# Optimization experiments

Hardware: AMD Instinct MI355X
Metric: run time of the kernel (lower is better)

Reference implementation:

```python
import jax, jax.numpy as jnp
import numpy as np

B, S, HID = 2, 2048, 2048
NH, NKV, HD = 16, 4, 128
G = NH // NKV  # kv group size
EPS = 1e-6


def setup_inputs() -> dict:
    key = jax.random.key(0)
    ks = jax.random.split(key, 7)
    w = 0.02
    return {
        "hidden_states": jax.random.normal(ks[0], (B, S, HID), dtype=jnp.float32),
        "position_ids": jnp.broadcast_to(jnp.arange(S, dtype=jnp.int64), (B, S)),
        "Wq": jax.random.normal(ks[1], (2 * NH * HD, HID), dtype=jnp.float32) * w,
        "Wk": jax.random.normal(ks[2], (NKV * HD, HID), dtype=jnp.float32) * w,
        "Wv": jax.random.normal(ks[3], (NKV * HD, HID), dtype=jnp.float32) * w,
        "Wo": jax.random.normal(ks[4], (HID, NH * HD), dtype=jnp.float32) * w,
        "norm_w": jnp.zeros((HID,), dtype=jnp.float32),
    }


def reference(hidden_states, position_ids, Wq, Wk, Wv, Wo, norm_w):
    # RMSNorm (weight parameterized as 1 + w, per source)
    ms = jnp.mean(hidden_states * hidden_states, axis=-1, keepdims=True)
    x = hidden_states * jax.lax.rsqrt(ms + EPS) * (1.0 + norm_w)

    qg = x @ Wq.T                                   # (B,S,2*NH*HD)
    q, gate = jnp.split(qg, 2, axis=-1)
    q = q.reshape(B, S, NH, HD).transpose(0, 2, 1, 3)       # (B,NH,S,HD)
    gate = gate.reshape(B, S, NH, HD).transpose(0, 2, 1, 3)
    k = (x @ Wk.T).reshape(B, S, NKV, HD).transpose(0, 2, 1, 3)  # (B,NKV,S,HD)
    v = (x @ Wv.T).reshape(B, S, NKV, HD).transpose(0, 2, 1, 3)

    scale = 1.0 / np.sqrt(HD).astype(np.float32)
    qg4 = q.reshape(B, NKV, G, S, HD)
    attn = jnp.einsum("bkgqd,bkld->bkgql", qg4, k) * scale   # (B,NKV,G,S,S)
    p = jax.nn.softmax(attn, axis=-1)
    o = jnp.einsum("bkgql,bkld->bkgqd", p, v).reshape(B, NH, S, HD)

    o = o * jax.nn.sigmoid(gate)                    # output gate
    o = o.transpose(0, 2, 1, 3).reshape(B, S, NH * HD)
    return o @ Wo.T
```

## Files before the change

kernel.cpp:

```cpp
#include <hip/hip_runtime.h>
#include <math.h>

#define BB    2
#define SS    2048
#define HIDD  2048
#define NHH   16
#define NKVV  4
#define HDD   128
#define MROWS 4096
#define QG_N  4096
#define KV_N  512
#define O_N   2048
#define KDIM  2048
#define EPS_  1e-6f
#define SCALE_ 0.08838834764831845f

typedef __attribute__((ext_vector_type(8))) __bf16 bf16x8;
typedef __attribute__((ext_vector_type(8))) unsigned short u16x8;
typedef __attribute__((ext_vector_type(4))) float f32x4;

__device__ __forceinline__ unsigned short f2bf(float f) {
  return __builtin_bit_cast(unsigned short, (__bf16)f);
}

__global__ __launch_bounds__(256) void f2bf_all(const float* __restrict__ Wq,
                                                const float* __restrict__ Wk,
                                                const float* __restrict__ Wv,
                                                const float* __restrict__ Wo,
                                                unsigned short* __restrict__ dst) {
  const int s0 = QG_N * KDIM / 4;
  const int s1 = s0 + KV_N * KDIM / 4;
  const int s2 = s1 + KV_N * KDIM / 4;
  const int s3 = s2 + O_N * KDIM / 4;
  int i = blockIdx.x * 256 + threadIdx.x;
  if (i >= s3) return;
  float4 v;
  if (i < s0)      v = ((const float4*)Wq)[i];
  else if (i < s1) v = ((const float4*)Wk)[i - s0];
  else if (i < s2) v = ((const float4*)Wv)[i - s1];
  else             v = ((const float4*)Wo)[i - s2];
  ushort4 u;
  u.x = f2bf(v.x); u.y = f2bf(v.y); u.z = f2bf(v.z); u.w = f2bf(v.w);
  ((ushort4*)dst)[i] = u;
}

__global__ __launch_bounds__(256) void rmsnorm_k(const float* __restrict__ h,
                                                 const float* __restrict__ w,
                                                 unsigned short* __restrict__ x) {
  int row = blockIdx.x;
  int t = threadIdx.x;
  const float4* hr = (const float4*)(h + (size_t)row * HIDD);
  const float4* w4 = (const float4*)w;

  float4 v0 = hr[t], v1 = hr[t + 256];
  float ss = v0.x*v0.x + v0.y*v0.y + v0.z*v0.z + v0.w*v0.w
           + v1.x*v1.x + v1.y*v1.y + v1.z*v1.z + v1.w*v1.w;
#pragma unroll
  for (int off = 32; off > 0; off >>= 1) ss += __shfl_down(ss, off, 64);

  __shared__ float part[4];
  __shared__ float rs_sh;
  if ((t & 63) == 0) part[t >> 6] = ss;
  __syncthreads();
  if (t == 0) rs_sh = rsqrtf((part[0]+part[1]+part[2]+part[3]) * (1.0f/HIDD) + EPS_);
  __syncthreads();
  float rs = rs_sh;

  float4 w0 = w4[t], w1 = w4[t + 256];
  ushort4 o0, o1;
  o0.x = f2bf(v0.x * rs * (1.f + w0.x));
  o0.y = f2bf(v0.y * rs * (1.f + w0.y));
  o0.z = f2bf(v0.z * rs * (1.f + w0.z));
  o0.w = f2bf(v0.w * rs * (1.f + w0.w));
  o1.x = f2bf(v1.x * rs * (1.f + w1.x));
  o1.y = f2bf(v1.y * rs * (1.f + w1.y));
  o1.z = f2bf(v1.z * rs * (1.f + w1.z));
  o1.w = f2bf(v1.w * rs * (1.f + w1.w));
  ushort4* xr = (ushort4*)(x + (size_t)row * HIDD);
  xr[t] = o0;
  xr[t + 256] = o1;
}

template <int OBF>
__device__ __forceinline__ void gemm_core(const unsigned short* __restrict__ Ab,
                                          const unsigned short* __restrict__ Bb,
                                          void* __restrict__ Cv,
                                          int Ndim, int bm, int bn,
                                          unsigned short* Als, unsigned short* Bls) {
  char* ldsA = (char*)Als;
  char* ldsB = (char*)Bls;

  int t   = threadIdx.x;
  int r15 = t & 15;
  int g   = (t & 63) >> 4;
  int w   = t >> 6;
  int wr  = w >> 1, wc = w & 1;

  f32x4 acc[4][4] = {};

  for (int k0 = 0; k0 < KDIM; k0 += 64) {
    __syncthreads();
#pragma unroll
    for (int it = 0; it < 4; ++it) {
      int f      = it * 256 + t;
      int row    = f >> 3;
      int schunk = (f & 7) ^ (row & 7);
      unsigned ldsbase = (unsigned)((it * 256 + (w << 6)) << 4);
      __builtin_amdgcn_global_load_lds(
          (const unsigned int*)(Ab + ((size_t)(bm + row) << 11) + k0 + schunk * 8),
          (unsigned int*)(ldsA + ldsbase), 16, 0, 0);
      __builtin_amdgcn_global_load_lds(
          (const unsigned int*)(Bb + ((size_t)(bn + row) << 11) + k0 + schunk * 8),
          (unsigned int*)(ldsB + ldsbase), 16, 0, 0);
    }
    __syncthreads();

#pragma unroll
    for (int tt = 0; tt < 2; ++tt) {
      bf16x8 af[4], bfv[4];
#pragma unroll
      for (int mi = 0; mi < 4; ++mi) {
        int row = wr * 64 + mi * 16 + r15;
        af[mi] = *(const bf16x8*)(ldsA + row * 128 + (((4 * tt + g) ^ (row & 7)) << 4));
      }
#pragma unroll
      for (int ni = 0; ni < 4; ++ni) {
        int row = wc * 64 + ni * 16 + r15;
        bfv[ni] = *(const bf16x8*)(ldsB + row * 128 + (((4 * tt + g) ^ (row & 7)) << 4));
      }
      __builtin_amdgcn_s_setprio(1);
#pragma unroll
      for (int mi = 0; mi < 4; ++mi)
#pragma unroll
        for (int ni = 0; ni < 4; ++ni)
          acc[mi][ni] = __builtin_amdgcn_mfma_f32_16x16x32_bf16(af[mi], bfv[ni], acc[mi][ni], 0, 0, 0);
      __builtin_amdgcn_s_setprio(0);
    }
  }

#pragma unroll
  for (int mi = 0; mi < 4; ++mi)
#pragma unroll
    for (int ni = 0; ni < 4; ++ni) {
      int col = bn + wc * 64 + ni * 16 + r15;
#pragma unroll
      for (int r = 0; r < 4; ++r) {
        int rowg = bm + wr * 64 + mi * 16 + g * 4 + r;
        if (OBF == 1)
          ((unsigned short*)Cv)[(size_t)rowg * Ndim + col] = f2bf(acc[mi][ni][r]);
        else if (OBF == 3) {
          int t6 = rowg & 63;
          int sig = (t6 & 32) + ((t6 & 12) << 1) + ((t6 & 16) >> 2) + (t6 & 3);
          int tokp = (rowg & ~63) | sig;
          ((unsigned short*)Cv)[(size_t)col * MROWS + tokp] = f2bf(acc[mi][ni][r]);
        } else
          ((float*)Cv)[(size_t)rowg * Ndim + col] = acc[mi][ni][r];
      }
    }
}

template <int OBF>
__global__ __launch_bounds__(256) void gemm_bf16(const unsigned short* __restrict__ Ab,
                                                 const unsigned short* __restrict__ Bb,
                                                 void* __restrict__ Cv,
                                                 int Ndim) {
  __shared__ unsigned short Als[128 * 64];
  __shared__ unsigned short Bls[128 * 64];
  gemm_core<OBF>(Ab, Bb, Cv, Ndim, blockIdx.y * 128, blockIdx.x * 128, Als, Bls);
}

__global__ __launch_bounds__(256) void gemm_kv(const unsigned short* __restrict__ Ab,
                                               const unsigned short* __restrict__ Wk,
                                               const unsigned short* __restrict__ Wv,
                                               unsigned short* __restrict__ Ck,
                                               unsigned short* __restrict__ Cvt) {
  __shared__ unsigned short Als[128 * 64];
  __shared__ unsigned short Bls[128 * 64];
  int bx = blockIdx.x;
  if (bx < 4)
    gemm_core<1>(Ab, Wk, (void*)Ck, KV_N, blockIdx.y * 128, bx * 128, Als, Bls);
  else
    gemm_core<3>(Ab, Wv, (void*)Cvt, KV_N, blockIdx.y * 128, (bx & 3) * 128, Als, Bls);
}

#define LD8(basep, r, x) \
  (*(const bf16x8*)((basep) + (size_t)(r) * 128 + ((((x) ^ ((r)&7))) << 4)))

#define STAGE_A(bufi, h, tk)                                                   \
  { _Pragma("unroll")                                                          \
    for (int c = 0; c < 2; ++c) {                                              \
      int f = c * 512 + t;                                                     \
      int rr = f >> 3;                                                         \
      int sc = (f & 7) ^ (rr & 7);                                             \
      __builtin_amdgcn_global_load_lds(                                        \
        (const unsigned int*)(Ab + ((size_t)(bm + (h)*128 + rr) << 11) + (tk)*64 + sc*8), \
        (unsigned int*)(lds8 + (bufi)*32768 + (h)*16384 + c*8192 + (w<<10)), 16, 0, 0); \
    } }

#define STAGE_B(bufi, h, tk)                                                   \
  { _Pragma("unroll")                                                          \
    for (int c = 0; c < 2; ++c) {                                              \
      int f = c * 512 + t;                                                     \
      int rr = f >> 3;                                                         \
      int sc = (f & 7) ^ (rr & 7);                                             \
      __builtin_amdgcn_global_load_lds(                                        \
        (const unsigned int*)(Bbp + ((size_t)(bn + (h)*128 + rr) << 11) + (tk)*64 + sc*8), \
        (unsigned int*)(lds8 + 65536 + (bufi)*32768 + (h)*16384 + c*8192 + (w<<10)), 16, 0, 0); \
    } }

#define RD_A(SRC, MIBASE)                                                      \
  { _Pragma("unroll")                                                          \
    for (int mi = 0; mi < 4; ++mi) {                                           \
      int rr = wr * 128 + ((MIBASE) + mi) * 16 + r15;                          \
      afr[mi][0] = LD8(SRC, rr, g);                                            \
      afr[mi][1] = LD8(SRC, rr, 4 + g);                                        \
    } }

#define RD_B(SRC, NIBASE, DST)                                                 \
  { _Pragma("unroll")                                                          \
    for (int ni = 0; ni < 2; ++ni) {                                           \
      int rr = wc * 64 + ((NIBASE) + ni) * 16 + r15;                           \
      DST[ni][0] = LD8(SRC, rr, g);                                            \
      DST[ni][1] = LD8(SRC, rr, 4 + g);                                        \
    } }

#define MFMA_QUAD(MIBASE, NIBASE, BREG)                                        \
  { __builtin_amdgcn_s_setprio(1);                                             \
    _Pragma("unroll")                                                          \
    for (int mi = 0; mi < 4; ++mi)                                             \
      _Pragma("unroll")                                                        \
      for (int ni = 0; ni < 2; ++ni)                                           \
        _Pragma("unroll")                                                      \
        for (int ks = 0; ks < 2; ++ks)                                         \
          acc[(MIBASE)+mi][(NIBASE)+ni] =                                      \
            __builtin_amdgcn_mfma_f32_16x16x32_bf16(afr[mi][ks], BREG[ni][ks], \
                                                    acc[(MIBASE)+mi][(NIBASE)+ni], 0, 0, 0); \
    __builtin_amdgcn_s_setprio(0); }

#define BAR() __builtin_amdgcn_s_barrier()

__global__ __launch_bounds__(512, 2) void gemm_qg256(const unsigned short* __restrict__ Ab,
                                                     const unsigned short* __restrict__ Bbp,
                                                     unsigned short* __restrict__ Cq,
                                                     float* __restrict__ Cg) {
  __shared__ char lds8[131072];
  int t = threadIdx.x;
  int r15 = t & 15, g = (t & 63) >> 4, w = t >> 6;
  int wr = w >> 2, wc = w & 3;
  int bm = blockIdx.y * 256, bn = blockIdx.x * 256;
  char* A0 = lds8;            char* A1 = lds8 + 32768;
  char* B0 = lds8 + 65536;    char* B1 = lds8 + 98304;

  f32x4 acc[8][4] = {};
  bf16x8 afr[4][2], b0r[2][2], b1r[2][2];

  STAGE_A(0, 0, 0); STAGE_A(0, 1, 0); STAGE_B(0, 0, 0); STAGE_B(0, 1, 0);
  STAGE_A(1, 0, 1); STAGE_A(1, 1, 1); STAGE_B(1, 0, 1); STAGE_B(1, 1, 1);
  asm volatile("s_waitcnt vmcnt(8)" ::: "memory");
  BAR();

  for (int i = 0; i < 15; ++i) {
    int te = 2 * i + 2, to = 2 * i + 3;
    RD_A(A0, 0); RD_B(B0, 0, b0r);
    BAR(); MFMA_QUAD(0, 0, b0r); BAR();
    RD_B(B0, 2, b1r);
    BAR(); MFMA_QUAD(0, 2, b1r); BAR();
    RD_A(A0, 4);
    STAGE_B(0, 0, te);
    BAR(); MFMA_QUAD(4, 0, b0r); BAR();
    STAGE_A(0, 0, te);
    BAR(); MFMA_QUAD(4, 2, b1r);
    asm volatile("s_waitcnt vmcnt(4)" ::: "memory");
    BAR();
    RD_A(A1, 0); RD_B(B1, 0, b0r);
    STAGE_A(0, 1, te);
    BAR(); MFMA_QUAD(0, 0, b0r); BAR();
    RD_B(B1, 2, b1r);
    STAGE_B(0, 1, te);
    BAR(); MFMA_QUAD(0, 2, b1r); BAR();
    RD_A(A1, 4);
    STAGE_B(1, 0, to); STAGE_B(1, 1, to);
    BAR(); MFMA_QUAD(4, 0, b0r); BAR();
    STAGE_A(1, 0, to); STAGE_A(1, 1, to);
    BAR(); MFMA_QUAD(4, 2, b1r);
    asm volatile("s_waitcnt vmcnt(8)" ::: "memory");
    BAR();
  }
  RD_A(A0, 0); RD_B(B0, 0, b0r);
  BAR(); MFMA_QUAD(0, 0, b0r); BAR();
  RD_B(B0, 2, b1r);
  BAR(); MFMA_QUAD(0, 2, b1r); BAR();
  RD_A(A0, 4);
  BAR(); MFMA_QUAD(4, 0, b0r); BAR();
  BAR(); MFMA_QUAD(4, 2, b1r);
  asm volatile("s_waitcnt vmcnt(0)" ::: "memory");
  BAR();
  RD_A(A1, 0); RD_B(B1, 0, b0r);
  BAR(); MFMA_QUAD(0, 0, b0r); BAR();
  RD_B(B1, 2, b1r);
  BAR(); MFMA_QUAD(0, 2, b1r); BAR();
  RD_A(A1, 4);
  BAR(); MFMA_QUAD(4, 0, b0r); BAR();
  BAR(); MFMA_QUAD(4, 2, b1r);

  bool isq = (bn < O_N);
  int colbase = bn + wc * 64;
#pragma unroll
  for (int mi = 0; mi < 8; ++mi) {
    size_t row = (size_t)bm + wr * 128 + mi * 16 + g * 4;
#pragma unroll
    for (int ni = 0; ni < 4; ++ni) {
      int col = colbase + ni * 16 + r15;
#pragma unroll
      for (int r = 0; r < 4; ++r) {
        if (isq) Cq[(row + r) * O_N + col] = f2bf(acc[mi][ni][r] * SCALE_);
        else     Cg[(row + r) * O_N + (col - O_N)] = acc[mi][ni][r];
      }
    }
  }
}

__global__ __launch_bounds__(256, 2) void attn_mfma(const unsigned short* __restrict__ qb,
                                                    const float* __restrict__ gateb,
                                                    const unsigned short* __restrict__ kb,
                                                    const unsigned short* __restrict__ vt,
                                                    unsigned short* __restrict__ obuf) {
  __shared__ unsigned short Ks[2][64 * 128];
  __shared__ unsigned short Vt[2][128 * 64];
  char* ldsK0 = (char*)Ks;
  char* ldsV0 = (char*)Vt;

  int t = threadIdx.x;
  int l = t & 63, w = t >> 6;
  int c15 = l & 15, g = l >> 4;
  int bid = blockIdx.x;
  int swz = (bid & 7) * 64 + (bid >> 3);
  int qt = swz & 15, h = (swz >> 4) & 15, b = swz >> 8;
  int kh = h >> 2;
  size_t rowQ0 = (size_t)b * SS + (size_t)qt * 128;
  size_t rowKbase = (size_t)b * SS;

  bf16x8 qf[2][4];
#pragma unroll
  for (int qi = 0; qi < 2; ++qi)
#pragma unroll
    for (int ks = 0; ks < 4; ++ks)
      qf[qi][ks] = *(const bf16x8*)(qb + (rowQ0 + w * 32 + qi * 16 + c15) * O_N
                                       + h * HDD + g * 8 + ks * 32);

  f32x4 accO[2][8] = {};
  float mrun[2] = {-INFINITY, -INFINITY};
  float lrun[2] = {0.f, 0.f};

#define ISSUE_K(bufi, kt_)                                                     \
  {                                                                            \
    size_t rowK0 = rowKbase + (size_t)(kt_) * 64;                              \
    _Pragma("unroll")                                                          \
    for (int it = 0; it < 4; ++it) {                                           \
      int f = it * 256 + t;                                                    \
      int kv = f >> 4;                                                         \
      int schunk = (f & 15) ^ (kv & 7);                                        \
      unsigned ldsbase = (unsigned)((it * 256 + (w << 6)) << 4);               \
      __builtin_amdgcn_global_load_lds(                                        \
          (const unsigned int*)(kb + (rowK0 + kv) * KV_N + kh * HDD + schunk * 8), \
          (unsigned int*)(ldsK0 + (bufi) * 16384 + ldsbase), 16, 0, 0);        \
    }                                                                          \
  }
#define ISSUE_VT(bufi, kt_)                                                    \
  {                                                                            \
    size_t tokbase = rowKbase + (size_t)(kt_) * 64;                            \
    _Pragma("unroll")                                                          \
    for (int it = 0; it < 4; ++it) {                                           \
      int f = it * 256 + t;                                                    \
      int row = f >> 3;                                                        \
      int schunk = (f & 7) ^ (row & 7);                                        \
      unsigned ldsbase = (unsigned)((it * 256 + (w << 6)) << 4);               \
      __builtin_amdgcn_global_load_lds(                                        \
          (const unsigned int*)(vt + (size_t)(kh * 128 + row) * MROWS + tokbase + schunk * 8), \
          (unsigned int*)(ldsV0 + (bufi) * 16384 + ldsbase), 16, 0, 0);        \
    }                                                                          \
  }

  ISSUE_K(0, 0);
  ISSUE_VT(0, 0);
  asm volatile("s_waitcnt vmcnt(0)" ::: "memory");
  __syncthreads();

  const int NT = SS / 64;
  for (int kt = 0; kt < NT; ++kt) {
    int cur = kt & 1, nxt = cur ^ 1;
    char* ldsK = ldsK0 + cur * 16384;
    char* ldsV = ldsV0 + cur * 16384;

    if (kt + 1 < NT) {
      ISSUE_K(nxt, kt + 1);
      ISSUE_VT(nxt, kt + 1);
    }

    f32x4 accS[2][4] = {};
    __builtin_amdgcn_s_setprio(1);
#pragma unroll
    for (int nf = 0; nf < 4; ++nf) {
      int kvr = nf * 16 + c15;
#pragma unroll
      for (int ks = 0; ks < 4; ++ks) {
        bf16x8 kf = *(const bf16x8*)(ldsK + kvr * 256 + ((((g + 4 * ks) ^ (kvr & 7)) << 4)));
#pragma unroll
        for (int qi = 0; qi < 2; ++qi)
          accS[qi][nf] = __builtin_amdgcn_mfma_f32_16x16x32_bf16(kf, qf[qi][ks], accS[qi][nf], 0, 0, 0);
      }
    }
    __builtin_amdgcn_s_setprio(0);

    float mt[2];
#pragma unroll
    for (int qi = 0; qi < 2; ++qi) {
      float m0 = fmaxf(fmaxf(accS[qi][0][0], accS[qi][0][1]), fmaxf(accS[qi][0][2], accS[qi][0][3]));
#pragma unroll
      for (int nf = 1; nf < 4; ++nf)
        m0 = fmaxf(m0, fmaxf(fmaxf(accS[qi][nf][0], accS[qi][nf][1]), fmaxf(accS[qi][nf][2], accS[qi][nf][3])));
      m0 = fmaxf(m0, __shfl_xor(m0, 16, 64));
      m0 = fmaxf(m0, __shfl_xor(m0, 32, 64));
      mt[qi] = m0;
    }

    bool safe = (mt[0] <= mrun[0] + 8.f) && (mt[1] <= mrun[1] + 8.f);
    if (!__all(safe)) {
#pragma unroll
      for (int qi = 0; qi < 2; ++qi) {
        float mnew = fmaxf(mrun[qi], mt[qi]);
        float al = __expf(mrun[qi] - mnew);
        mrun[qi] = mnew;
        lrun[qi] *= al;
        float alr[4];
#pragma unroll
        for (int r = 0; r < 4; ++r) alr[r] = __shfl(al, g * 4 + r, 16);
#pragma unroll
        for (int df = 0; df < 8; ++df)
#pragma unroll
          for (int r = 0; r < 4; ++r) accO[qi][df][r] *= alr[r];
      }
    }

    u16x8 pfr[2][2];
#pragma unroll
    for (int qi = 0; qi < 2; ++qi) {
      float ps = 0.f;
#pragma unroll
      for (int nf = 0; nf < 4; ++nf) {
        float p0 = __expf(accS[qi][nf][0] - mrun[qi]);
        float p1 = __expf(accS[qi][nf][1] - mrun[qi]);
        float p2 = __expf(accS[qi][nf][2] - mrun[qi]);
        float p3 = __expf(accS[qi][nf][3] - mrun[qi]);
        ps += (p0 + p1) + (p2 + p3);
        pfr[qi][nf >> 1][(nf & 1) * 4 + 0] = f2bf(p0);
        pfr[qi][nf >> 1][(nf & 1) * 4 + 1] = f2bf(p1);
        pfr[qi][nf >> 1][(nf & 1) * 4 + 2] = f2bf(p2);
        pfr[qi][nf >> 1][(nf & 1) * 4 + 3] = f2bf(p3);
      }
      ps += __shfl_xor(ps, 16, 64);
      ps += __shfl_xor(ps, 32, 64);
      lrun[qi] += ps;
    }

    __builtin_amdgcn_s_setprio(1);
#pragma unroll
    for (int ks2 = 0; ks2 < 2; ++ks2) {
      bf16x8 pf0 = __builtin_bit_cast(bf16x8, pfr[0][ks2]);
      bf16x8 pf1 = __builtin_bit_cast(bf16x8, pfr[1][ks2]);
#pragma unroll
      for (int df = 0; df < 8; ++df) {
        int d = df * 16 + c15;
        bf16x8 vf = *(const bf16x8*)(ldsV + d * 128 + ((((g + 4 * ks2) ^ (d & 7)) << 4)));
        accO[0][df] = __builtin_amdgcn_mfma_f32_16x16x32_bf16(pf0, vf, accO[0][df], 0, 0, 0);
        accO[1][df] = __builtin_amdgcn_mfma_f32_16x16x32_bf16(pf1, vf, accO[1][df], 0, 0, 0);
      }
    }
    __builtin_amdgcn_s_setprio(0);

    if (kt + 1 < NT) {
      asm volatile("s_waitcnt vmcnt(0)" ::: "memory");
    }
    __syncthreads();
  }

#pragma unroll
  for (int qi = 0; qi < 2; ++qi) {
    float invL = 1.f / lrun[qi];
    float ivr[4];
#pragma unroll
    for (int r = 0; r < 4; ++r) ivr[r] = __shfl(invL, g * 4 + r, 16);
#pragma unroll
    for (int r = 0; r < 4; ++r) {
      size_t row = rowQ0 + w * 32 + qi * 16 + g * 4 + r;
#pragma unroll
      for (int df = 0; df < 8; ++df) {
        int d = df * 16 + c15;
        float gt = gateb[row * (size_t)O_N + h * HDD + d];
        float sg = 1.f / (1.f + __expf(-gt));
        obuf[row * (size_t)O_N + h * HDD + d] = f2bf(accO[qi][df][r] * ivr[r] * sg);
      }
    }
  }
#undef ISSUE_K
#undef ISSUE_VT
}

extern "C" void kernel_launch(void* const* d_in, const int* in_sizes, int n_in,
                              void* d_out, int out_size, void* d_ws, size_t ws_size,
                              hipStream_t stream) {
  const float* hs = (const float*)d_in[0];
  const float* Wq = (const float*)d_in[2];
  const float* Wk = (const float*)d_in[3];
  const float* Wv = (const float*)d_in[4];
  const float* Wo = (const float*)d_in[5];
  const float* nw = (const float*)d_in[6];
  float* out = (float*)d_out;

  float* gateb = (float*)d_ws;
  unsigned short* qb16 = (unsigned short*)(gateb + (size_t)MROWS * O_N);
  unsigned short* kb16 = qb16 + (size_t)MROWS * O_N;
  unsigned short* vt16 = kb16 + (size_t)MROWS * KV_N;
  unsigned short* xb   = vt16 + (size_t)KV_N * MROWS;
  unsigned short* ob   = xb   + (size_t)MROWS * HIDD;
  unsigned short* wqb  = ob   + (size_t)MROWS * O_N;
  unsigned short* wkb  = wqb  + (size_t)QG_N * KDIM;
  unsigned short* wvb  = wkb  + (size_t)KV_N * KDIM;
  unsigned short* wob  = wvb  + (size_t)KV_N * KDIM;

  const int tot4 = (QG_N + KV_N + KV_N + O_N) * KDIM / 4;
  f2bf_all<<<(tot4 + 255) / 256, 256, 0, stream>>>(Wq, Wk, Wv, Wo, wqb);
  rmsnorm_k<<<MROWS, 256, 0, stream>>>(hs, nw, xb);

  gemm_qg256<<<dim3(QG_N/256, MROWS/256), 512, 0, stream>>>(xb, wqb, qb16, gateb);
  gemm_kv<<<dim3(8, MROWS/128), 256, 0, stream>>>(xb, wkb, wvb, kb16, vt16);
  attn_mfma<<<dim3(512), 256, 0, stream>>>(qb16, gateb, kb16, vt16, ob);
  gemm_bf16<0><<<dim3(O_N/128, MROWS/128), 256, 0, stream>>>(ob, wob, out, O_N);
}
```

Before: 252.1 us.

## Replace output projection GEMM with 256x128 pipelined direct-to-LDS kernel

Replaces the generic 128x128 bf16 GEMM used for the output projection with a dedicated 512-thread kernel computing 256x128 tiles. It stages A and B tiles through global_load_lds into swizzled, double-buffered LDS and interleaves the next tile's loads with MFMA work, using setprio around the MFMA bursts. The goal is better data reuse per block and hiding of global memory latency, which is the same scheme the QG projection kernel uses. The trade-offs are halving the block count to 256 blocks and hand-tuned vmcnt waits, which must stay correct for the 32 K-steps.

```diff
diff --git a/kernel.cpp b/kernel.cpp
--- a/kernel.cpp
+++ b/kernel.cpp
@@ -320,6 +320,120 @@
   }
 }
 
+#define OST_A(bufi, h, tk)                                                     \
+  { _Pragma("unroll")                                                          \
+    for (int c = 0; c < 2; ++c) {                                              \
+      int f = c * 512 + t;                                                     \
+      int rr = f >> 3;                                                         \
+      int sc = (f & 7) ^ (rr & 7);                                             \
+      __builtin_amdgcn_global_load_lds(                                        \
+        (const unsigned int*)(Ab + ((size_t)(bm + (h)*128 + rr) << 11) + (tk)*64 + sc*8), \
+        (unsigned int*)(lds8 + (bufi)*32768 + (h)*16384 + c*8192 + (w<<10)), 16, 0, 0); \
+    } }
+
+#define OST_B(bufi, tk)                                                        \
+  { _Pragma("unroll")                                                          \
+    for (int c = 0; c < 2; ++c) {                                              \
+      int f = c * 512 + t;                                                     \
+      int rr = f >> 3;                                                         \
+      int sc = (f & 7) ^ (rr & 7);                                             \
+      __builtin_amdgcn_global_load_lds(                                        \
+        (const unsigned int*)(Bbp + ((size_t)(bn + rr) << 11) + (tk)*64 + sc*8), \
+        (unsigned int*)(lds8 + 65536 + (bufi)*16384 + c*8192 + (w<<10)), 16, 0, 0); \
+    } }
+
+#define ORD_A(bufi)                                                            \
+  { const char* abase = lds8 + (bufi)*32768 + (wr >> 1)*16384;                 \
+    _Pragma("unroll")                                                          \
+    for (int mi = 0; mi < 4; ++mi) {                                           \
+      int rl = ((wr & 1) * 64) + mi * 16 + r15;                                \
+      afr[mi][0] = LD8(abase, rl, g);                                          \
+      afr[mi][1] = LD8(abase, rl, 4 + g);                                      \
+    } }
+
+#define ORD_B(bufi, NIBASE, DST)                                               \
+  { const char* bbase = lds8 + 65536 + (bufi)*16384;                           \
+    _Pragma("unroll")                                                          \
+    for (int ni = 0; ni < 2; ++ni) {                                           \
+      int rl = wc * 64 + ((NIBASE) + ni) * 16 + r15;                           \
+      DST[ni][0] = LD8(bbase, rl, g);                                          \
+      DST[ni][1] = LD8(bbase, rl, 4 + g);                                      \
+    } }
+
+#define OMFMA(NIBASE, BREG)                                                    \
+  { __builtin_amdgcn_s_setprio(1);                                             \
+    _Pragma("unroll")                                                          \
+    for (int mi = 0; mi < 4; ++mi)                                             \
+      _Pragma("unroll")                                                        \
+      for (int ni = 0; ni < 2; ++ni)                                           \
+        _Pragma("unroll")                                                      \
+        for (int ks = 0; ks < 2; ++ks)                                         \
+          acc[mi][(NIBASE)+ni] =                                               \
+            __builtin_amdgcn_mfma_f32_16x16x32_bf16(afr[mi][ks], BREG[ni][ks], \
+                                                    acc[mi][(NIBASE)+ni], 0, 0, 0); \
+    __builtin_amdgcn_s_setprio(0); }
+
+__global__ __launch_bounds__(512, 2) void gemm_o256(const unsigned short* __restrict__ Ab,
+                                                    const unsigned short* __restrict__ Bbp,
+                                                    float* __restrict__ C) {
+  __shared__ char lds8[98304];
+  int t = threadIdx.x;
+  int r15 = t & 15, g = (t & 63) >> 4, w = t >> 6;
+  int wr = w >> 1, wc = w & 1;
+  int bm = blockIdx.y * 256, bn = blockIdx.x * 128;
+
+  f32x4 acc[4][4] = {};
+  bf16x8 afr[4][2], b0r[2][2], b1r[2][2];
+
+  OST_A(0, 0, 0); OST_A(0, 1, 0); OST_B(0, 0);
+  OST_A(1, 0, 1); OST_A(1, 1, 1);
+  asm volatile("s_waitcnt vmcnt(4)" ::: "memory");
+  BAR();
+
+  for (int i = 0; i < 15; ++i) {
+    int to = 2 * i + 1, te2 = 2 * i + 2, to2 = 2 * i + 3;
+    ORD_A(0); ORD_B(0, 0, b0r);
+    OST_B(1, to);
+    BAR(); OMFMA(0, b0r); BAR();
+    ORD_B(0, 2, b1r);
+    OST_A(0, 0, te2);
+    BAR(); OMFMA(2, b1r);
+    asm volatile("s_waitcnt vmcnt(2)" ::: "memory");
+    BAR();
+    ORD_A(1); ORD_B(1, 0, b0r);
+    OST_A(0, 1, te2); OST_B(0, te2);
+    BAR(); OMFMA(0, b0r); BAR();
+    ORD_B(1, 2, b1r);
+    OST_A(1, 0, to2); OST_A(1, 1, to2);
+    BAR(); OMFMA(2, b1r);
+    asm volatile("s_waitcnt vmcnt(4)" ::: "memory");
+    BAR();
+  }
+  ORD_A(0); ORD_B(0, 0, b0r);
+  OST_B(1, 31);
+  BAR(); OMFMA(0, b0r); BAR();
+  ORD_B(0, 2, b1r);
+  BAR(); OMFMA(2, b1r);
+  asm volatile("s_waitcnt vmcnt(0)" ::: "memory");
+  BAR();
+  ORD_A(1); ORD_B(1, 0, b0r);
+  BAR(); OMFMA(0, b0r); BAR();
+  ORD_B(1, 2, b1r);
+  BAR(); OMFMA(2, b1r);
+
+#pragma unroll
+  for (int mi = 0; mi < 4; ++mi) {
+    size_t row = (size_t)bm + wr * 64 + mi * 16 + g * 4;
+#pragma unroll
+    for (int ni = 0; ni < 4; ++ni) {
+      int col = bn + wc * 64 + ni * 16 + r15;
+#pragma unroll
+      for (int r = 0; r < 4; ++r)
+        C[(row + r) * O_N + col] = acc[mi][ni][r];
+    }
+  }
+}
+
 __global__ __launch_bounds__(256, 2) void attn_mfma(const unsigned short* __restrict__ qb,
                                                     const float* __restrict__ gateb,
                                                     const unsigned short* __restrict__ kb,
@@ -535,5 +649,5 @@
   gemm_qg256<<<dim3(QG_N/256, MROWS/256), 512, 0, stream>>>(xb, wqb, qb16, gateb);
   gemm_kv<<<dim3(8, MROWS/128), 256, 0, stream>>>(xb, wkb, wvb, kb16, vt16);
   attn_mfma<<<dim3(512), 256, 0, stream>>>(qb16, gateb, kb16, vt16, ob);
-  gemm_bf16<0><<<dim3(O_N/128, MROWS/128), 256, 0, stream>>>(ob, wob, out, O_N);
-}
+  gemm_o256<<<dim3(O_N/128, MROWS/256), 512, 0, stream>>>(ob, wob, out);
+}
```

Result: no change. 250.7 us (-0.6%).
